# Optimization experiments

Hardware: AMD Instinct MI355X
Metric: run time of the kernel (lower is better)

The kernel has to match this reference:

```python
import jax, jax.numpy as jnp
import numpy as np

LN_EPS = 1e-5
L1_EPS = 1e-12  # F.normalize clamp_min eps


def _layernorm(h, g, b):
    mu = h.mean(-1, keepdims=True)
    var = ((h - mu) ** 2).mean(-1, keepdims=True)
    return (h - mu) * jax.lax.rsqrt(var + LN_EPS) * g + b


def _graph(x, wq_w, wq_b, wk_w, wk_b, gcn_w, ln_g, ln_b):
    # x: [..., n, d]
    qx = x @ wq_w.T + wq_b
    kx = x @ wk_w.T + wk_b
    dot = jnp.einsum('...nd,...md->...nm', qx, kx)
    sq = dot * dot
    adj = sq / jnp.maximum(sq.sum(-1, keepdims=True), L1_EPS)  # L1-normalized rows
    for i in range(gcn_w.shape[0]):
        h = adj @ (x @ gcn_w[i])
        x = jax.nn.relu(_layernorm(h, ln_g[i], ln_b[i]))
    return x.mean(-2)  # mean over nodes -> [..., d]


def setup_inputs() -> dict:
    key = jax.random.key(0)
    ks = jax.random.split(key, 12)
    N, FR, B, NF = 16, 32, 50, 768
    L, NC = 2, 400
    s = 1.0 / np.sqrt(NF)
    inp = {
        'feats': jax.random.normal(ks[0], (N, FR, B, NF), jnp.float32),
        'feat_global_single': jax.random.normal(ks[1], (N, NF), jnp.float32),
        'feat_single_previous': jax.random.normal(ks[2], (N, NF), jnp.float32),
        'wq_w': jax.random.normal(ks[3], (NF, NF), jnp.float32) * s,
        'wq_b': jnp.zeros((NF,), jnp.float32),
        'wk_w': jax.random.normal(ks[4], (NF, NF), jnp.float32) * s,
        'wk_b': jnp.zeros((NF,), jnp.float32),
        'gcn_w': jax.random.normal(ks[5], (L, NF, NF), jnp.float32) * s,
        'ln_g': jnp.ones((L, NF), jnp.float32),
        'ln_b': jnp.zeros((L, NF), jnp.float32),
        'fc1_w': jax.random.normal(ks[6], (NF, 2 * NF), jnp.float32) / np.sqrt(2 * NF),
        'fc1_b': jnp.zeros((NF,), jnp.float32),
        'fc2_w': jax.random.normal(ks[7], (NC, NF), jnp.float32) * s,
        'fc2_b': jnp.zeros((NC,), jnp.float32),
        't_c': 0,
    }
    return inp


def reference(feats, feat_global_single, feat_single_previous,
              wq_w, wq_b, wk_w, wk_b, gcn_w, ln_g, ln_b,
              fc1_w, fc1_b, fc2_w, fc2_b, t_c):
    N, FR, B, NF = feats.shape
    x = feats.reshape(N * FR, B, NF)
    # object-level graph (shared weights)
    x = _graph(x, wq_w, wq_b, wk_w, wk_b, gcn_w, ln_g, ln_b)  # [N*FR, NF]
    x = x.reshape(N, FR, NF)
    # frame-level graph (same shared weights)
    x = _graph(x, wq_w, wq_b, wk_w, wk_b, gcn_w, ln_g, ln_b)  # [N, NF]
    y = jnp.concatenate([x, feat_global_single], axis=-1)      # [N, 2*NF]
    # ClassifierSimple (dropout = identity in eval)
    h = jax.nn.relu(y @ fc1_w.T + fc1_b)
    logits = h @ fc2_w.T + fc2_b
    return (logits, y)
```

## Files before the change

kernel.cpp:

```cpp
#include <hip/hip_runtime.h>
#include <hip/hip_bf16.h>

typedef unsigned short u16;
typedef unsigned int   u32;
typedef __attribute__((ext_vector_type(8))) short short8;
typedef __attribute__((ext_vector_type(4))) float float4v;

__device__ __forceinline__ float bf2f(u16 u){ union{u32 i; float f;} c; c.i = ((u32)u) << 16; return c.f; }
__device__ __forceinline__ float bflo(u32 u){ union{u32 i; float f;} c; c.i = u << 16; return c.f; }
__device__ __forceinline__ float bfhi(u32 u){ union{u32 i; float f;} c; c.i = u & 0xFFFF0000u; return c.f; }
__device__ __forceinline__ u16 f2bf(float f){
  union{float f; u32 i;} c; c.f = f; u32 x = c.i;
  return (u16)((x + 0x7FFFu + ((x >> 16) & 1u)) >> 16);
}
__device__ __forceinline__ u32 pack2(float a, float b){
  union { __hip_bfloat162 h; u32 u; } c;
  c.h = __float22bfloat162_rn(float2{a, b});
  return c.u;
}

__device__ __forceinline__ void async16(const void* g, void* l){
  __builtin_amdgcn_global_load_lds((const __attribute__((address_space(1))) void*)g,
                                   (__attribute__((address_space(3))) void*)l, 16, 0, 0);
}

__global__ void prep_qkw(const float* __restrict__ wq, const float* __restrict__ wk,
                         const float* __restrict__ wqb, const float* __restrict__ wkb,
                         u16* __restrict__ QHB, float* __restrict__ biasQH)
{
  int t = blockIdx.x * 256 + threadIdx.x;
  int stride = gridDim.x * 256;
  for (int i = t; i < 294912; i += stride) {
    float4 v = (i < 147456) ? ((const float4*)wq)[i] : ((const float4*)wk)[i - 147456];
    ushort4 o; o.x = f2bf(v.x); o.y = f2bf(v.y); o.z = f2bf(v.z); o.w = f2bf(v.w);
    ((ushort4*)QHB)[i] = o;
  }
  if (t < 768) biasQH[t] = wqb[t];
  else if (t < 1536) biasQH[t] = wkb[t - 768];
  else if (t < 2304) biasQH[t] = 0.f;
}

__global__ void prep_gcnT(const float* __restrict__ gcn, u16* __restrict__ QHB, u16* __restrict__ gcnT1)
{
  __shared__ float tile[32][33];
  int l = blockIdx.z;
  int d0 = blockIdx.y * 32, o0 = blockIdx.x * 32;
  int tx = threadIdx.x, ty = threadIdx.y;
  const float* src = gcn + (size_t)l * 589824;
  u16* dst = (l == 0) ? (QHB + (size_t)1536 * 768) : gcnT1;
  for (int i = 0; i < 32; i += 8) tile[ty + i][tx] = src[(size_t)(d0 + ty + i) * 768 + o0 + tx];
  __syncthreads();
  for (int i = 0; i < 32; i += 8) dst[(size_t)(o0 + ty + i) * 768 + d0 + tx] = f2bf(tile[tx][ty + i]);
}

template<bool AF32>
__global__ void __launch_bounds__(256) gemm_bt(const void* __restrict__ Aptr, const u16* __restrict__ Bw,
                                               const float* __restrict__ bias, u16* __restrict__ C,
                                               int M, int N, int K)
{
  __shared__ __attribute__((aligned(16))) u16 As[128 * 32];
  __shared__ __attribute__((aligned(16))) u16 Bs[128 * 32];
  int tid = threadIdx.x, lane = tid & 63, wid = tid >> 6;
  int wm = wid >> 1, wn = wid & 1;
  size_t m0 = (size_t)blockIdx.y * 128, n0 = (size_t)blockIdx.x * 128;

  float4v acc[4][4];
  for (int r = 0; r < 4; r++) for (int c = 0; c < 4; c++) acc[r][c] = (float4v){0.f, 0.f, 0.f, 0.f};

  int srow = 32 * wid + (lane >> 2);
  int sq   = (lane & 3) ^ ((lane >> 3) & 3);
  const u16*  gB  = Bw + (n0 + srow) * (size_t)K + sq * 8;
  u16* lB = &Bs[1024 * wid];
  const float* gAf0 = AF32 ? ((const float*)Aptr + (m0 + srow) * (size_t)K + sq * 8) : nullptr;
  const float* gAf1 = AF32 ? ((const float*)Aptr + (m0 + srow + 16) * (size_t)K + sq * 8) : nullptr;
  const u16*  gA16 = AF32 ? nullptr : ((const u16*)Aptr + (m0 + srow) * (size_t)K + sq * 8);
  u16* lA = &As[1024 * wid];
  int wslot16 = srow * 32 + (lane & 3) * 8;

  int l15 = lane & 15;
  int rs  = (lane >> 4) ^ ((lane >> 1) & 3);

  for (int kt = 0; kt < K; kt += 32) {
    if (AF32) {
      float4 f0 = *(const float4*)(gAf0 + kt);
      float4 f1 = *(const float4*)(gAf0 + kt + 4);
      float4 f2 = *(const float4*)(gAf1 + kt);
      float4 f3 = *(const float4*)(gAf1 + kt + 4);
      async16(gB + kt, lB);
      async16(gB + kt + (size_t)16 * K, lB + 512);
      uint4 o0 = { pack2(f0.x,f0.y), pack2(f0.z,f0.w), pack2(f1.x,f1.y), pack2(f1.z,f1.w) };
      uint4 o1 = { pack2(f2.x,f2.y), pack2(f2.z,f2.w), pack2(f3.x,f3.y), pack2(f3.z,f3.w) };
      *(uint4*)&As[wslot16]            = o0;
      *(uint4*)&As[wslot16 + 16 * 32]  = o1;
    } else {
      async16(gA16 + kt, lA);
      async16(gA16 + kt + (size_t)16 * K, lA + 512);
      async16(gB + kt, lB);
      async16(gB + kt + (size_t)16 * K, lB + 512);
    }
    __syncthreads();
    short8 af[4], bfr[4];
    for (int r = 0; r < 4; r++) af[r]  = *(const short8*)&As[(wm * 64 + r * 16 + l15) * 32 + rs * 8];
    for (int c = 0; c < 4; c++) bfr[c] = *(const short8*)&Bs[(wn * 64 + c * 16 + l15) * 32 + rs * 8];
    for (int r = 0; r < 4; r++)
      for (int c = 0; c < 4; c++)
        acc[r][c] = __builtin_amdgcn_mfma_f32_16x16x32_bf16(af[r], bfr[c], acc[r][c], 0, 0, 0);
    __syncthreads();
  }

  int quad = lane >> 4;
  for (int c = 0; c < 4; c++) {
    int n = (int)n0 + wn * 64 + c * 16 + l15;
    float bv = bias ? bias[n] : 0.f;
    for (int r = 0; r < 4; r++) {
      size_t mbase = m0 + wm * 64 + r * 16 + quad * 4;
      for (int t = 0; t < 4; t++)
        C[(mbase + t) * (size_t)N + n] = f2bf(acc[r][c][t] + bv);
    }
  }
}


template<int NP>
__global__ void __launch_bounds__(512) fused_l1(const u16* __restrict__ QH,
                                                const float* __restrict__ lng, const float* __restrict__ lnb,
                                                u16* __restrict__ adjG, u16* __restrict__ X, int n)
{
  constexpr int ST = 72;
  constexpr int TPW = (NP == 64) ? 2 : 1;
  __shared__ __attribute__((aligned(16))) u16 adjb[NP * ST];
  __shared__ __attribute__((aligned(16))) u16 HT[64 * ST];
  __shared__ float rsum[NP];
  __shared__ float stats[NP][2];
  __shared__ float bc[NP][2];
  __shared__ float lg[768], lb[768];

  int g = blockIdx.x;
  int tid = threadIdx.x, lane = tid & 63, w = tid >> 6;
  int l15 = lane & 15, quad = lane >> 4;

  for (int i = tid; i < 768; i += 512) { lg[i] = lng[i]; lb[i] = lnb[i]; }
  if (tid < NP) { rsum[tid] = 0.f; stats[tid][0] = 0.f; stats[tid][1] = 0.f; }
  __syncthreads();

  int mt, nt0; bool s_act;
  if (NP == 64) { mt = w & 3; nt0 = (w >> 2) * 2; s_act = true; }
  else          { mt = w & 1; nt0 = w >> 1;       s_act = (w < 4); }

  int rowA = mt * 16 + l15;
  bool aok = rowA < n;
  const u16* pA  = QH + ((size_t)g * n + rowA) * 2304 + quad * 8;
  int rowB0 = (nt0) * 16 + l15, rowB1 = (nt0 + TPW - 1) * 16 + l15;
  bool b0ok = rowB0 < n, b1ok = rowB1 < n;
  const u16* pB0 = QH + ((size_t)g * n + rowB0) * 2304 + 768 + quad * 8;
  const u16* pB1 = QH + ((size_t)g * n + rowB1) * 2304 + 768 + quad * 8;

  float4v sacc[TPW];
  for (int j = 0; j < TPW; j++) sacc[j] = (float4v){0.f, 0.f, 0.f, 0.f};

  if (s_act) {
    for (int kt = 0; kt < 768; kt += 32) {
      uint4 av = {0,0,0,0}, bv0 = {0,0,0,0}, bv1 = {0,0,0,0};
      if (aok)  av  = *(const uint4*)(pA + kt);
      if (b0ok) bv0 = *(const uint4*)(pB0 + kt);
      if (TPW == 2 && b1ok) bv1 = *(const uint4*)(pB1 + kt);
      short8 a = *(short8*)&av;
      sacc[0] = __builtin_amdgcn_mfma_f32_16x16x32_bf16(a, *(short8*)&bv0, sacc[0], 0, 0, 0);
      if (TPW == 2)
        sacc[1] = __builtin_amdgcn_mfma_f32_16x16x32_bf16(a, *(short8*)&bv1, sacc[1], 0, 0, 0);
    }
    for (int t = 0; t < 4; t++) {
      float s = 0.f;
      for (int j = 0; j < TPW; j++) { float v = sacc[j][t]; s += v * v; }
      s += __shfl_xor(s, 1); s += __shfl_xor(s, 2); s += __shfl_xor(s, 4); s += __shfl_xor(s, 8);
      if (l15 == 0) atomicAdd(&rsum[mt * 16 + quad * 4 + t], s);
    }
  }
  __syncthreads();
  if (tid < NP) rsum[tid] = 1.0f / fmaxf(rsum[tid], 1e-12f);
  __syncthreads();
  if (s_act) {
    u16* gadj = adjG + (size_t)g * NP * NP;
    for (int j = 0; j < TPW; j++)
      for (int t = 0; t < 4; t++) {
        int row = mt * 16 + quad * 4 + t, col = (nt0 + j) * 16 + l15;
        float v = sacc[j][t];
        u16 b = f2bf(v * v * rsum[row]);
        adjb[row * ST + col] = b;
        gadj[row * NP + col] = b;
      }
  }
  __syncthreads();

  int m2, nt20;
  if (NP == 64) { m2 = w & 3; nt20 = (w >> 2) * 2; }
  else          { m2 = w & 1; nt20 = w >> 1; }

  float4v xacc[12][TPW];
#pragma unroll
  for (int ch = 0; ch < 12; ch++) for (int j = 0; j < TPW; j++) xacc[ch][j] = (float4v){0.f,0.f,0.f,0.f};

  int hj  = tid & (NP - 1);
  int hseg= (NP == 64) ? w : ((tid >> 5) & 7);
  bool hact = (NP == 64) ? true : (tid < NP * 8);

#pragma unroll
  for (int ch = 0; ch < 12; ch++) {
    uint4 hv = {0,0,0,0};
    if (hact && hj < n) hv = *(const uint4*)(QH + ((size_t)g * n + hj) * 2304 + 1536 + ch * 64 + hseg * 8);
    __syncthreads();
    if (hact) {
      const u16* ep = (const u16*)&hv;
      for (int i = 0; i < 8; i++) HT[(hseg * 8 + i) * ST + hj] = ep[i];
    }
    __syncthreads();
    for (int k = 0; k < NP / 32; k++) {
      short8 a = *(const short8*)&adjb[(m2 * 16 + l15) * ST + k * 32 + quad * 8];
      for (int j = 0; j < TPW; j++) {
        short8 b = *(const short8*)&HT[((nt20 + j) * 16 + l15) * ST + k * 32 + quad * 8];
        xacc[ch][j] = __builtin_amdgcn_mfma_f32_16x16x32_bf16(a, b, xacc[ch][j], 0, 0, 0);
      }
    }
  }

  float ssum[4] = {0,0,0,0}, ssq[4] = {0,0,0,0};
#pragma unroll
  for (int ch = 0; ch < 12; ch++)
    for (int j = 0; j < TPW; j++)
      for (int t = 0; t < 4; t++) { float v = xacc[ch][j][t]; ssum[t] += v; ssq[t] += v * v; }
  for (int m = 1; m <= 8; m <<= 1)
    for (int t = 0; t < 4; t++) { ssum[t] += __shfl_xor(ssum[t], m); ssq[t] += __shfl_xor(ssq[t], m); }
  if (l15 == 0)
    for (int t = 0; t < 4; t++) {
      atomicAdd(&stats[m2 * 16 + quad * 4 + t][0], ssum[t]);
      atomicAdd(&stats[m2 * 16 + quad * 4 + t][1], ssq[t]);
    }
  __syncthreads();
  if (tid < NP) {
    float mu = stats[tid][0] * (1.f / 768.f);
    float var = stats[tid][1] * (1.f / 768.f) - mu * mu;
    bc[tid][0] = mu; bc[tid][1] = rsqrtf(fmaxf(var, 0.f) + 1e-5f);
  }
  __syncthreads();

#pragma unroll
  for (int ch = 0; ch < 12; ch++)
    for (int j = 0; j < TPW; j++)
      for (int t = 0; t < 4; t++) {
        int row = m2 * 16 + quad * 4 + t;
        if (row < n) {
          int d = ch * 64 + (nt20 + j) * 16 + l15;
          float v = fmaxf((xacc[ch][j][t] - bc[row][0]) * bc[row][1] * lg[d] + lb[d], 0.f);
          X[((size_t)g * n + row) * 768 + d] = f2bf(v);
        }
      }
}

template<int NP>
__global__ void __launch_bounds__(512) fused_l2(const u16* __restrict__ adjG, const u16* __restrict__ H,
                                                const float* __restrict__ lng, const float* __restrict__ lnb,
                                                u16* __restrict__ Xmean, int n, float inv)
{
  constexpr int ST = 72;
  constexpr int TPW = (NP == 64) ? 2 : 1;
  __shared__ __attribute__((aligned(16))) u16 adjb[NP * ST];
  __shared__ __attribute__((aligned(16))) u16 HT[64 * ST];
  __shared__ float stats[NP][2];
  __shared__ float bc[NP][2];
  __shared__ float colsum[768];
  __shared__ float lg[768], lb[768];

  int g = blockIdx.x;
  int tid = threadIdx.x, lane = tid & 63, w = tid >> 6;
  int l15 = lane & 15, quad = lane >> 4;

  for (int i = tid; i < 768; i += 512) { lg[i] = lng[i]; lb[i] = lnb[i]; colsum[i] = 0.f; }
  if (tid < NP) { stats[tid][0] = 0.f; stats[tid][1] = 0.f; }
  if (tid * 8 < NP * NP) {
    int row = (tid * 8) / NP, c0 = (tid * 8) % NP;
    uint4 v = *(const uint4*)(adjG + (size_t)g * NP * NP + row * NP + c0);
    *(uint4*)&adjb[row * ST + c0] = v;
  }

  int m2, nt20;
  if (NP == 64) { m2 = w & 3; nt20 = (w >> 2) * 2; }
  else          { m2 = w & 1; nt20 = w >> 1; }

  float4v xacc[12][TPW];
#pragma unroll
  for (int ch = 0; ch < 12; ch++) for (int j = 0; j < TPW; j++) xacc[ch][j] = (float4v){0.f,0.f,0.f,0.f};

  int hj  = tid & (NP - 1);
  int hseg= (NP == 64) ? w : ((tid >> 5) & 7);
  bool hact = (NP == 64) ? true : (tid < NP * 8);

#pragma unroll
  for (int ch = 0; ch < 12; ch++) {
    uint4 hv = {0,0,0,0};
    if (hact && hj < n) hv = *(const uint4*)(H + ((size_t)g * n + hj) * 768 + ch * 64 + hseg * 8);
    __syncthreads();
    if (hact) {
      const u16* ep = (const u16*)&hv;
      for (int i = 0; i < 8; i++) HT[(hseg * 8 + i) * ST + hj] = ep[i];
    }
    __syncthreads();
    for (int k = 0; k < NP / 32; k++) {
      short8 a = *(const short8*)&adjb[(m2 * 16 + l15) * ST + k * 32 + quad * 8];
      for (int j = 0; j < TPW; j++) {
        short8 b = *(const short8*)&HT[((nt20 + j) * 16 + l15) * ST + k * 32 + quad * 8];
        xacc[ch][j] = __builtin_amdgcn_mfma_f32_16x16x32_bf16(a, b, xacc[ch][j], 0, 0, 0);
      }
    }
  }

  float ssum[4] = {0,0,0,0}, ssq[4] = {0,0,0,0};
#pragma unroll
  for (int ch = 0; ch < 12; ch++)
    for (int j = 0; j < TPW; j++)
      for (int t = 0; t < 4; t++) { float v = xacc[ch][j][t]; ssum[t] += v; ssq[t] += v * v; }
  for (int m = 1; m <= 8; m <<= 1)
    for (int t = 0; t < 4; t++) { ssum[t] += __shfl_xor(ssum[t], m); ssq[t] += __shfl_xor(ssq[t], m); }
  if (l15 == 0)
    for (int t = 0; t < 4; t++) {
      atomicAdd(&stats[m2 * 16 + quad * 4 + t][0], ssum[t]);
      atomicAdd(&stats[m2 * 16 + quad * 4 + t][1], ssq[t]);
    }
  __syncthreads();
  if (tid < NP) {
    float mu = stats[tid][0] * (1.f / 768.f);
    float var = stats[tid][1] * (1.f / 768.f) - mu * mu;
    bc[tid][0] = mu; bc[tid][1] = rsqrtf(fmaxf(var, 0.f) + 1e-5f);
  }
  __syncthreads();

#pragma unroll
  for (int ch = 0; ch < 12; ch++)
    for (int j = 0; j < TPW; j++)
      for (int t = 0; t < 4; t++) {
        int row = m2 * 16 + quad * 4 + t;
        int d = ch * 64 + (nt20 + j) * 16 + l15;
        float v = fmaxf((xacc[ch][j][t] - bc[row][0]) * bc[row][1] * lg[d] + lb[d], 0.f);
        float vm = (row < n) ? v : 0.f;
        vm += __shfl_xor(vm, 16);
        vm += __shfl_xor(vm, 32);
        if (quad == 0) atomicAdd(&colsum[d], vm);
      }
  __syncthreads();
  if (tid < 384)
    ((u32*)Xmean)[(size_t)g * 384 + tid] = pack2(colsum[tid * 2] * inv, colsum[tid * 2 + 1] * inv);
}

__global__ void __launch_bounds__(384) concat_y(const u16* __restrict__ Xm,
                                                const float* __restrict__ fgs, float* __restrict__ yout)
{
  int b = blockIdx.x, tid = threadIdx.x;
  u32 u = ((const u32*)Xm)[(size_t)b * 384 + tid];
  int d0 = tid * 2;
  yout[(size_t)b * 1536 + d0]     = bflo(u);
  yout[(size_t)b * 1536 + d0 + 1] = bfhi(u);
  yout[(size_t)b * 1536 + 768 + d0]     = fgs[(size_t)b * 768 + d0];
  yout[(size_t)b * 1536 + 768 + d0 + 1] = fgs[(size_t)b * 768 + d0 + 1];
}

__global__ void __launch_bounds__(256) fc1_relu(const float* __restrict__ yout,
                                                const float* __restrict__ fc1w, const float* __restrict__ fc1b,
                                                float* __restrict__ h)
{
  int o = blockIdx.x * 4 + (threadIdx.x >> 6);
  int lane = threadIdx.x & 63;
  float acc[16];
  for (int b = 0; b < 16; b++) acc[b] = 0.f;
  const float4* wr = (const float4*)(fc1w + (size_t)o * 1536);
  for (int k4 = lane; k4 < 384; k4 += 64) {
    float4 wv = wr[k4];
    for (int b = 0; b < 16; b++) {
      float4 yv = ((const float4*)(yout + (size_t)b * 1536))[k4];
      acc[b] += wv.x * yv.x + wv.y * yv.y + wv.z * yv.z + wv.w * yv.w;
    }
  }
  for (int m = 1; m <= 32; m <<= 1)
    for (int b = 0; b < 16; b++) acc[b] += __shfl_xor(acc[b], m);
  if (lane < 16) h[(size_t)lane * 768 + o] = fmaxf(acc[lane] + fc1b[o], 0.f);
}

__global__ void __launch_bounds__(256) fc2_out(const float* __restrict__ h,
                                               const float* __restrict__ fc2w, const float* __restrict__ fc2b,
                                               float* __restrict__ logits)
{
  int o = blockIdx.x * 4 + (threadIdx.x >> 6);
  int lane = threadIdx.x & 63;
  float acc[16];
  for (int b = 0; b < 16; b++) acc[b] = 0.f;
  const float4* wr = (const float4*)(fc2w + (size_t)o * 768);
  for (int k4 = lane; k4 < 192; k4 += 64) {
    float4 wv = wr[k4];
    for (int b = 0; b < 16; b++) {
      float4 hv = ((const float4*)(h + (size_t)b * 768))[k4];
      acc[b] += wv.x * hv.x + wv.y * hv.y + wv.z * hv.z + wv.w * hv.w;
    }
  }
  for (int m = 1; m <= 32; m <<= 1)
    for (int b = 0; b < 16; b++) acc[b] += __shfl_xor(acc[b], m);
  if (lane < 16) logits[(size_t)lane * 400 + o] = acc[lane] + fc2b[o];
}

extern "C" void kernel_launch(void* const* d_in, const int* in_sizes, int n_in,
                              void* d_out, int out_size, void* d_ws, size_t ws_size,
                              hipStream_t stream) {
  const float* feats = (const float*)d_in[0];
  const float* fgs   = (const float*)d_in[1];
  const float* wq_w  = (const float*)d_in[3];
  const float* wq_b  = (const float*)d_in[4];
  const float* wk_w  = (const float*)d_in[5];
  const float* wk_b  = (const float*)d_in[6];
  const float* gcn_w = (const float*)d_in[7];
  const float* ln_g  = (const float*)d_in[8];
  const float* ln_b  = (const float*)d_in[9];
  const float* fc1_w = (const float*)d_in[10];
  const float* fc1_b = (const float*)d_in[11];
  const float* fc2_w = (const float*)d_in[12];
  const float* fc2_b = (const float*)d_in[13];
  float* out  = (float*)d_out;
  float* yout = out + 16 * 400;

  char* ws = (char*)d_ws;
  size_t off = 0;
  auto alloc = [&](size_t b){ size_t r = off; off = (off + b + 255) & ~(size_t)255; return r; };
  u16*  QHB    = (u16*) (ws + alloc((size_t)2304 * 768 * 2));
  u16*  gcnT1  = (u16*) (ws + alloc((size_t)768 * 768 * 2));
  float* biasQH= (float*)(ws + alloc((size_t)2304 * 4));
  u16*  Xf     = (u16*) (ws + alloc((size_t)512 * 768 * 2));
  u16*  QHf    = (u16*) (ws + alloc((size_t)512 * 2304 * 2));
  u16*  X1f    = (u16*) (ws + alloc((size_t)512 * 768 * 2));
  u16*  H2f    = (u16*) (ws + alloc((size_t)512 * 768 * 2));
  u16*  adjFb  = (u16*) (ws + alloc((size_t)16 * 32 * 32 * 2));
  u16*  Xm     = (u16*) (ws + alloc((size_t)16 * 768 * 2));
  float* hbuf  = (float*)(ws + alloc((size_t)16 * 768 * 4));
  size_t base = off;

  auto need = [&](int GC){
    size_t R = (size_t)GC * 50;
    return base + R * 2304 * 2 + 512 + R * 768 * 2 + 512 + (size_t)GC * 64 * 64 * 2 + 512;
  };
  int GC = 64;
  if (need(512) <= ws_size) GC = 512;
  else if (need(256) <= ws_size) GC = 256;
  else if (need(128) <= ws_size) GC = 128;
  int R = GC * 50;
  size_t off2 = base;
  auto alloc2 = [&](size_t b){ size_t r = off2; off2 = (off2 + b + 255) & ~(size_t)255; return r; };
  u16* QHc   = (u16*)(ws + alloc2((size_t)R * 2304 * 2));
  u16* X1c   = (u16*)(ws + alloc2((size_t)R * 768 * 2));
  u16* adjGc = (u16*)(ws + alloc2((size_t)GC * 64 * 64 * 2));
  u16* H2c   = QHc;

  prep_qkw<<<288, 256, 0, stream>>>(wq_w, wk_w, wq_b, wk_b, QHB, biasQH);
  prep_gcnT<<<dim3(24, 24, 2), dim3(32, 8), 0, stream>>>(gcn_w, QHB, gcnT1);

  int nchunks = 512 / GC;
  for (int c = 0; c < nchunks; c++) {
    const float* fc = feats + (size_t)c * GC * 50 * 768;
    gemm_bt<true><<<dim3(18, R / 128), 256, 0, stream>>>(fc, QHB, biasQH, QHc, R, 2304, 768);
    fused_l1<64><<<GC, 512, 0, stream>>>(QHc, ln_g, ln_b, adjGc, X1c, 50);
    gemm_bt<false><<<dim3(6, R / 128), 256, 0, stream>>>(X1c, gcnT1, nullptr, H2c, R, 768, 768);
    fused_l2<64><<<GC, 512, 0, stream>>>(adjGc, H2c, ln_g + 768, ln_b + 768,
                                         Xf + (size_t)c * GC * 768, 50, 1.f / 50.f);
  }

  gemm_bt<false><<<dim3(18, 4), 256, 0, stream>>>(Xf, QHB, biasQH, QHf, 512, 2304, 768);
  fused_l1<32><<<16, 512, 0, stream>>>(QHf, ln_g, ln_b, adjFb, X1f, 32);
  gemm_bt<false><<<dim3(6, 4), 256, 0, stream>>>(X1f, gcnT1, nullptr, H2f, 512, 768, 768);
  fused_l2<32><<<16, 512, 0, stream>>>(adjFb, H2f, ln_g + 768, ln_b + 768, Xm, 32, 1.f / 32.f);

  concat_y<<<16, 384, 0, stream>>>(Xm, fgs, yout);
  fc1_relu<<<192, 256, 0, stream>>>(yout, fc1_w, fc1_b, hbuf);
  fc2_out<<<100, 256, 0, stream>>>(hbuf, fc2_w, fc2_b, out);
}
```

Before: 595.6 us.

## Pre-convert feats to bf16 and deepen GEMM K-tile to 64 with swizzle

Adds a standalone pass that converts the whole fp32 feats tensor to bf16, so the GEMM loads A through async global-to-LDS copies instead of converting in registers. The GEMM K-step doubles to 64, with a new XOR swizzle, halving the number of barrier pairs per tile. The grid is transposed so consecutive blocks walk along M and share the same weight tile. The cost is an extra full read and write of the ~79MB input plus a 39MB workspace buffer.

```diff
diff --git a/kernel.cpp b/kernel.cpp
--- a/kernel.cpp
+++ b/kernel.cpp
@@ -22,6 +22,18 @@
 __device__ __forceinline__ void async16(const void* g, void* l){
   __builtin_amdgcn_global_load_lds((const __attribute__((address_space(1))) void*)g,
                                    (__attribute__((address_space(3))) void*)l, 16, 0, 0);
+}
+
+__global__ void __launch_bounds__(256) conv_bf16(const float* __restrict__ src, u16* __restrict__ dst, int n8)
+{
+  int t = blockIdx.x * 256 + threadIdx.x;
+  int stride = gridDim.x * 256;
+  for (int i = t; i < n8; i += stride) {
+    float4 a = ((const float4*)src)[2 * i];
+    float4 b = ((const float4*)src)[2 * i + 1];
+    uint4 o = { pack2(a.x, a.y), pack2(a.z, a.w), pack2(b.x, b.y), pack2(b.z, b.w) };
+    ((uint4*)dst)[i] = o;
+  }
 }
 
 __global__ void prep_qkw(const float* __restrict__ wq, const float* __restrict__ wk,
@@ -53,67 +65,65 @@
   for (int i = 0; i < 32; i += 8) dst[(size_t)(o0 + ty + i) * 768 + d0 + tx] = f2bf(tile[tx][ty + i]);
 }
 
-template<bool AF32>
-__global__ void __launch_bounds__(256) gemm_bt(const void* __restrict__ Aptr, const u16* __restrict__ Bw,
+__global__ void __launch_bounds__(256) gemm_bt(const u16* __restrict__ A, const u16* __restrict__ Bw,
                                                const float* __restrict__ bias, u16* __restrict__ C,
                                                int M, int N, int K)
 {
-  __shared__ __attribute__((aligned(16))) u16 As[128 * 32];
-  __shared__ __attribute__((aligned(16))) u16 Bs[128 * 32];
+  __shared__ __attribute__((aligned(16))) u16 As[128 * 64];
+  __shared__ __attribute__((aligned(16))) u16 Bs[128 * 64];
   int tid = threadIdx.x, lane = tid & 63, wid = tid >> 6;
   int wm = wid >> 1, wn = wid & 1;
-  size_t m0 = (size_t)blockIdx.y * 128, n0 = (size_t)blockIdx.x * 128;
+  size_t m0 = (size_t)blockIdx.x * 128, n0 = (size_t)blockIdx.y * 128;
 
   float4v acc[4][4];
   for (int r = 0; r < 4; r++) for (int c = 0; c < 4; c++) acc[r][c] = (float4v){0.f, 0.f, 0.f, 0.f};
 
-  int srow = 32 * wid + (lane >> 2);
-  int sq   = (lane & 3) ^ ((lane >> 3) & 3);
-  const u16*  gB  = Bw + (n0 + srow) * (size_t)K + sq * 8;
-  u16* lB = &Bs[1024 * wid];
-  const float* gAf0 = AF32 ? ((const float*)Aptr + (m0 + srow) * (size_t)K + sq * 8) : nullptr;
-  const float* gAf1 = AF32 ? ((const float*)Aptr + (m0 + srow + 16) * (size_t)K + sq * 8) : nullptr;
-  const u16*  gA16 = AF32 ? nullptr : ((const u16*)Aptr + (m0 + srow) * (size_t)K + sq * 8);
-  u16* lA = &As[1024 * wid];
-  int wslot16 = srow * 32 + (lane & 3) * 8;
-
-  int l15 = lane & 15;
-  int rs  = (lane >> 4) ^ ((lane >> 1) & 3);
-
-  for (int kt = 0; kt < K; kt += 32) {
-    if (AF32) {
-      float4 f0 = *(const float4*)(gAf0 + kt);
-      float4 f1 = *(const float4*)(gAf0 + kt + 4);
-      float4 f2 = *(const float4*)(gAf1 + kt);
-      float4 f3 = *(const float4*)(gAf1 + kt + 4);
-      async16(gB + kt, lB);
-      async16(gB + kt + (size_t)16 * K, lB + 512);
-      uint4 o0 = { pack2(f0.x,f0.y), pack2(f0.z,f0.w), pack2(f1.x,f1.y), pack2(f1.z,f1.w) };
-      uint4 o1 = { pack2(f2.x,f2.y), pack2(f2.z,f2.w), pack2(f3.x,f3.y), pack2(f3.z,f3.w) };
-      *(uint4*)&As[wslot16]            = o0;
-      *(uint4*)&As[wslot16 + 16 * 32]  = o1;
-    } else {
-      async16(gA16 + kt, lA);
-      async16(gA16 + kt + (size_t)16 * K, lA + 512);
-      async16(gB + kt, lB);
-      async16(gB + kt + (size_t)16 * K, lB + 512);
-    }
-    __syncthreads();
-    short8 af[4], bfr[4];
-    for (int r = 0; r < 4; r++) af[r]  = *(const short8*)&As[(wm * 64 + r * 16 + l15) * 32 + rs * 8];
-    for (int c = 0; c < 4; c++) bfr[c] = *(const short8*)&Bs[(wn * 64 + c * 16 + l15) * 32 + rs * 8];
-    for (int r = 0; r < 4; r++)
-      for (int c = 0; c < 4; c++)
-        acc[r][c] = __builtin_amdgcn_mfma_f32_16x16x32_bf16(af[r], bfr[c], acc[r][c], 0, 0, 0);
-    __syncthreads();
-  }
-
-  int quad = lane >> 4;
+  int srow8  = lane >> 3;
+  int schunk = (lane & 7) ^ srow8;
+  const u16* gA[4]; const u16* gB[4];
+  u16* lA[4]; u16* lB[4];
+#pragma unroll
+  for (int j = 0; j < 4; j++) {
+    int r = 32 * wid + 8 * j + srow8;
+    gA[j] = A  + (m0 + r) * (size_t)K + schunk * 8;
+    gB[j] = Bw + (n0 + r) * (size_t)K + schunk * 8;
+    lA[j] = &As[(32 * wid + 8 * j) * 64];
+    lB[j] = &Bs[(32 * wid + 8 * j) * 64];
+  }
+
+  int l15 = lane & 15, quad = lane >> 4;
+  int s0 = quad ^ (l15 & 7);
+
+  for (int kt = 0; kt < K; kt += 64) {
+#pragma unroll
+    for (int j = 0; j < 4; j++) {
+      async16(gA[j] + kt, lA[j]);
+      async16(gB[j] + kt, lB[j]);
+    }
+    __syncthreads();
+#pragma unroll
+    for (int ks = 0; ks < 2; ks++) {
+      int so = (s0 ^ (ks << 2)) * 8;
+      short8 af[4], bfr[4];
+#pragma unroll
+      for (int r = 0; r < 4; r++) af[r]  = *(const short8*)&As[(wm * 64 + r * 16 + l15) * 64 + so];
+#pragma unroll
+      for (int c = 0; c < 4; c++) bfr[c] = *(const short8*)&Bs[(wn * 64 + c * 16 + l15) * 64 + so];
+#pragma unroll
+      for (int r = 0; r < 4; r++)
+#pragma unroll
+        for (int c = 0; c < 4; c++)
+          acc[r][c] = __builtin_amdgcn_mfma_f32_16x16x32_bf16(af[r], bfr[c], acc[r][c], 0, 0, 0);
+    }
+    __syncthreads();
+  }
+
+  int quad4 = quad * 4;
   for (int c = 0; c < 4; c++) {
     int n = (int)n0 + wn * 64 + c * 16 + l15;
     float bv = bias ? bias[n] : 0.f;
     for (int r = 0; r < 4; r++) {
-      size_t mbase = m0 + wm * 64 + r * 16 + quad * 4;
+      size_t mbase = m0 + wm * 64 + r * 16 + quad4;
       for (int t = 0; t < 4; t++)
         C[(mbase + t) * (size_t)N + n] = f2bf(acc[r][c][t] + bv);
     }
@@ -429,6 +439,7 @@
   u16*  QHB    = (u16*) (ws + alloc((size_t)2304 * 768 * 2));
   u16*  gcnT1  = (u16*) (ws + alloc((size_t)768 * 768 * 2));
   float* biasQH= (float*)(ws + alloc((size_t)2304 * 4));
+  u16*  Abf    = (u16*) (ws + alloc((size_t)25600 * 768 * 2));
   u16*  Xf     = (u16*) (ws + alloc((size_t)512 * 768 * 2));
   u16*  QHf    = (u16*) (ws + alloc((size_t)512 * 2304 * 2));
   u16*  X1f    = (u16*) (ws + alloc((size_t)512 * 768 * 2));
@@ -454,22 +465,23 @@
   u16* adjGc = (u16*)(ws + alloc2((size_t)GC * 64 * 64 * 2));
   u16* H2c   = QHc;
 
+  conv_bf16<<<2048, 256, 0, stream>>>(feats, Abf, 25600 * 768 / 8);
   prep_qkw<<<288, 256, 0, stream>>>(wq_w, wk_w, wq_b, wk_b, QHB, biasQH);
   prep_gcnT<<<dim3(24, 24, 2), dim3(32, 8), 0, stream>>>(gcn_w, QHB, gcnT1);
 
   int nchunks = 512 / GC;
   for (int c = 0; c < nchunks; c++) {
-    const float* fc = feats + (size_t)c * GC * 50 * 768;
-    gemm_bt<true><<<dim3(18, R / 128), 256, 0, stream>>>(fc, QHB, biasQH, QHc, R, 2304, 768);
+    const u16* fc = Abf + (size_t)c * GC * 50 * 768;
+    gemm_bt<<<dim3(R / 128, 18), 256, 0, stream>>>(fc, QHB, biasQH, QHc, R, 2304, 768);
     fused_l1<64><<<GC, 512, 0, stream>>>(QHc, ln_g, ln_b, adjGc, X1c, 50);
-    gemm_bt<false><<<dim3(6, R / 128), 256, 0, stream>>>(X1c, gcnT1, nullptr, H2c, R, 768, 768);
+    gemm_bt<<<dim3(R / 128, 6), 256, 0, stream>>>(X1c, gcnT1, nullptr, H2c, R, 768, 768);
     fused_l2<64><<<GC, 512, 0, stream>>>(adjGc, H2c, ln_g + 768, ln_b + 768,
                                          Xf + (size_t)c * GC * 768, 50, 1.f / 50.f);
   }
 
-  gemm_bt<false><<<dim3(18, 4), 256, 0, stream>>>(Xf, QHB, biasQH, QHf, 512, 2304, 768);
+  gemm_bt<<<dim3(4, 18), 256, 0, stream>>>(Xf, QHB, biasQH, QHf, 512, 2304, 768);
   fused_l1<32><<<16, 512, 0, stream>>>(QHf, ln_g, ln_b, adjFb, X1f, 32);
-  gemm_bt<false><<<dim3(6, 4), 256, 0, stream>>>(X1f, gcnT1, nullptr, H2f, 512, 768, 768);
+  gemm_bt<<<dim3(4, 6), 256, 0, stream>>>(X1f, gcnT1, nullptr, H2f, 512, 768, 768);
   fused_l2<32><<<16, 512, 0, stream>>>(adjFb, H2f, ln_g + 768, ln_b + 768, Xm, 32, 1.f / 32.f);
 
   concat_y<<<16, 384, 0, stream>>>(Xm, fgs, yout);
```

After: 521.3 us. 1.14x faster.
